# Kernel optimization log

Hardware: AMD Instinct MI355X
Metric: run time of the kernel (lower is better)

Reference implementation:

```python
import jax, jax.numpy as jnp
import numpy as np

BN_EPS = 1e-5


def setup_inputs() -> dict:
    key = jax.random.key(0)
    ks = jax.random.split(key, 16)
    N, E = 50000, 800000
    IN, OUT, EA, EE = 128, 128, 32, 16
    s = lambda k, fi, fo: jax.random.normal(k, (fi, fo), jnp.float32) / np.sqrt(fi)
    return {
        "x": jax.random.normal(ks[0], (N, IN), jnp.float32),
        "edge_attr": jax.random.normal(ks[1], (E, EA), jnp.float32),
        "W_emb": s(ks[2], EA, EE), "b_emb": jnp.zeros((EE,), jnp.float32),
        "W_temb": s(ks[3], EE, OUT), "b_temb": jnp.zeros((OUT,), jnp.float32),
        "W_tattr": s(ks[4], EA, OUT), "b_tattr": jnp.zeros((OUT,), jnp.float32),
        "W_gate": s(ks[5], 3 * OUT, OUT), "b_gate": jnp.zeros((OUT,), jnp.float32),
        "W_l": s(ks[6], IN, OUT), "b_l": jnp.zeros((OUT,), jnp.float32),
        "W_r": s(ks[7], IN, OUT),
        "gamma": jnp.ones((OUT,), jnp.float32), "beta": jnp.zeros((OUT,), jnp.float32),
        "edge_index": jax.random.randint(ks[8], (2, E), 0, N, jnp.int64 if jax.config.jax_enable_x64 else jnp.int32),
    }


def reference(x, edge_attr, W_emb, b_emb, W_temb, b_temb, W_tattr, b_tattr,
              W_gate, b_gate, W_l, b_l, W_r, gamma, beta, edge_index):
    N = x.shape[0]
    row, col = edge_index[0], edge_index[1]

    # edge feature transforms
    emb = jax.nn.relu(edge_attr @ W_emb + b_emb)          # [E, EE]
    t_attr = edge_attr @ W_tattr + b_tattr                # [E, OUT]
    t = (emb @ W_temb + b_temb) + t_attr                  # [E, OUT]

    # SAGEConv (PyG default): mean-aggregate source feats x[row] at target col
    agg = jax.ops.segment_sum(x[row], col, num_segments=N)           # [N, IN]
    cnt = jax.ops.segment_sum(jnp.ones_like(col, x.dtype), col, num_segments=N)
    agg = agg / jnp.maximum(cnt, 1.0)[:, None]
    out = agg @ W_l + b_l + x @ W_r                       # [N, OUT]

    # edge gating: gather out at targets, gate, scatter-add back
    comb = jnp.concatenate([out[col], t, t_attr], axis=-1)  # [E, 3*OUT]
    gate = jax.nn.sigmoid(comb @ W_gate + b_gate)           # [E, OUT]
    out = out + jax.ops.segment_sum(gate * t, col, num_segments=N)

    # BatchNorm1d (training-mode batch stats, biased variance)
    mu = jnp.mean(out, axis=0)
    var = jnp.mean((out - mu) ** 2, axis=0)
    out = (out - mu) * jax.lax.rsqrt(var + BN_EPS) * gamma + beta

    # residual = Identity -> out + out, then relu
    return jax.nn.relu(2.0 * out)
```

## Files before the change

kernel.cpp:

```cpp
#include <hip/hip_runtime.h>
#include <math.h>

#define BN_EPS 1e-5f

typedef short s16x8 __attribute__((ext_vector_type(8)));
typedef float f32x4 __attribute__((ext_vector_type(4)));
#define MFMA16(a, b, c) __builtin_amdgcn_mfma_f32_16x16x32_bf16(a, b, c, 0, 0, 0)

static __device__ __forceinline__ short f2b(float f) {
  union { float f; unsigned u; } x;
  x.f = f;
  unsigned r = (x.u + 0x7fffu + ((x.u >> 16) & 1u)) >> 16;
  return (short)r;
}
static __device__ __forceinline__ float b2f(unsigned bits16) {
  union { unsigned u; float f; } x;
  x.u = bits16 << 16;
  return x.f;
}

__global__ __launch_bounds__(256) void k_prep(
    const float* __restrict__ We, const float* __restrict__ Wta,
    const float* __restrict__ Wte, const float* __restrict__ Wg,
    const float* __restrict__ bta, const float* __restrict__ bte,
    const float* __restrict__ bg,
    short* __restrict__ WembT, short* __restrict__ WtaT,
    short* __restrict__ WteT, short* __restrict__ B1,
    short* __restrict__ B23, short* __restrict__ Bem,
    float* __restrict__ bgf) {
  int t = blockIdx.x * 256 + threadIdx.x;
  if (t < 512) {
    int c = t >> 5, k = t & 31;
    WembT[t] = f2b(We[k * 16 + c]);
  }
  if (t < 4096) {
    int c = t >> 5, k = t & 31;
    WtaT[t] = f2b(Wta[k * 128 + c]);
    WteT[t] = (k < 16) ? f2b(Wte[k * 128 + c]) : (short)0;
  }
  if (t < 16384) {
    int c = t >> 7, k = t & 127;
    B1[t] = f2b(Wg[k * 128 + c]);
    B23[t] = f2b(Wg[(128 + k) * 128 + c] + Wg[(256 + k) * 128 + c]);
  }
  if (t < 4096) {
    int c = t >> 5, k = t & 31;
    float s = 0.f;
    if (k < 16)
      for (int j = 0; j < 128; ++j) s += Wte[k * 128 + j] * Wg[(128 + j) * 128 + c];
    Bem[t] = (k < 16) ? f2b(s) : (short)0;
  }
  if (t < 128) {
    float s = bg[t];
    for (int j = 0; j < 128; ++j)
      s += (bta[j] + bte[j]) * Wg[(128 + j) * 128 + t] +
           bta[j] * Wg[(256 + j) * 128 + t];
    bgf[t] = s;
  }
}

__global__ __launch_bounds__(256) void k_count(
    const int* __restrict__ ei, int* __restrict__ cnt, int E) {
  for (int e = blockIdx.x * blockDim.x + threadIdx.x; e < E;
       e += gridDim.x * blockDim.x)
    atomicAdd(&cnt[ei[E + e]], 1);
}

__global__ __launch_bounds__(1024) void k_scan(
    const int* __restrict__ cnt, int* __restrict__ rowptr,
    int* __restrict__ wo, int N) {
  __shared__ int s[1024];
  __shared__ int carry_s;
  int tid = threadIdx.x;
  if (tid == 0) { carry_s = 0; rowptr[0] = 0; }
  __syncthreads();
  for (int base = 0; base < N; base += 1024) {
    int i = base + tid;
    int v = (i < N) ? cnt[i] : 0;
    s[tid] = v;
    __syncthreads();
#pragma unroll
    for (int off = 1; off < 1024; off <<= 1) {
      int t = (tid >= off) ? s[tid - off] : 0;
      __syncthreads();
      s[tid] += t;
      __syncthreads();
    }
    int inc = s[tid] + carry_s;
    if (i < N) { rowptr[i + 1] = inc; wo[i] = inc - v; }
    __syncthreads();
    if (tid == 1023) carry_s = inc;
    __syncthreads();
  }
}

__global__ __launch_bounds__(256) void k_fill(
    const int* __restrict__ ei, int* __restrict__ wo,
    int* __restrict__ src, int* __restrict__ inv, int E) {
  for (int e = blockIdx.x * blockDim.x + threadIdx.x; e < E;
       e += gridDim.x * blockDim.x) {
    int c = ei[E + e];
    int p = atomicAdd(&wo[c], 1);
    src[p] = ei[e];
    inv[e] = p;
  }
}

__global__ __launch_bounds__(256) void k_agg_gather(
    const float* __restrict__ x, const int* __restrict__ rowptr,
    const int* __restrict__ src, float* __restrict__ agg, int N) {
  int node = blockIdx.x * 4 + (threadIdx.x >> 6);
  if (node >= N) return;
  int l = threadIdx.x & 63;
  int s0 = rowptr[node], s1 = rowptr[node + 1];
  float a0 = 0.f, a1 = 0.f;
  int i = s0;
  for (; i + 1 < s1; i += 2) {
    int sa = src[i], sb = src[i + 1];
    float2 va = reinterpret_cast<const float2*>(x + (size_t)sa * 128)[l];
    float2 vb = reinterpret_cast<const float2*>(x + (size_t)sb * 128)[l];
    a0 += va.x + vb.x;
    a1 += va.y + vb.y;
  }
  if (i < s1) {
    float2 va = reinterpret_cast<const float2*>(x + (size_t)src[i] * 128)[l];
    a0 += va.x;
    a1 += va.y;
  }
  float sc = 1.0f / fmaxf((float)(s1 - s0), 1.0f);
  float2 r = make_float2(a0 * sc, a1 * sc);
  reinterpret_cast<float2*>(agg + (size_t)node * 128)[l] = r;
}

__global__ __launch_bounds__(256) void k_aggregate(
    const float* __restrict__ x, const int* __restrict__ ei,
    float* __restrict__ agg, float* __restrict__ cnt, int N, int E) {
  int total = E * 32;
  for (int idx = blockIdx.x * blockDim.x + threadIdx.x; idx < total;
       idx += gridDim.x * blockDim.x) {
    int e = idx >> 5, c = idx & 31;
    int r = ei[e];
    int d = ei[E + e];
    float4 v = reinterpret_cast<const float4*>(x)[(size_t)r * 32 + c];
    float* dst = agg + (size_t)d * 128 + c * 4;
    unsafeAtomicAdd(dst + 0, v.x);
    unsafeAtomicAdd(dst + 1, v.y);
    unsafeAtomicAdd(dst + 2, v.z);
    unsafeAtomicAdd(dst + 3, v.w);
    if (c == 0) unsafeAtomicAdd(cnt + d, 1.0f);
  }
}

__global__ __launch_bounds__(256) void k_node_linear(
    const float* __restrict__ x, float* __restrict__ agg,
    const float* __restrict__ cntf, const float* __restrict__ Wl,
    const float* __restrict__ bl, const float* __restrict__ Wr,
    float* __restrict__ out_lin, int N, int csr) {
  __shared__ float a_s[32][128];
  __shared__ float x_s[32][128];
  int n0 = blockIdx.x * 32;
  int tid = threadIdx.x;
#pragma unroll
  for (int i = 0; i < 16; ++i) {
    int idx = tid + i * 256;
    int nl = idx >> 7, j = idx & 127;
    int n = n0 + nl;
    float av = 0.f, xv = 0.f;
    if (n < N) {
      size_t off = (size_t)n * 128 + j;
      if (csr) {
        av = agg[off];
      } else {
        av = agg[off] / fmaxf(cntf[n], 1.0f);
        agg[off] = 0.0f;
      }
      xv = x[off];
    }
    a_s[nl][j] = av;
    x_s[nl][j] = xv;
  }
  __syncthreads();
  int j = tid & 127, g = tid >> 7;
  float acc[16];
  float bj = bl[j];
#pragma unroll
  for (int i = 0; i < 16; ++i) acc[i] = bj;
  for (int k = 0; k < 128; ++k) {
    float wl = Wl[k * 128 + j];
    float wr = Wr[k * 128 + j];
#pragma unroll
    for (int i = 0; i < 16; ++i)
      acc[i] += a_s[g * 16 + i][k] * wl + x_s[g * 16 + i][k] * wr;
  }
#pragma unroll
  for (int i = 0; i < 16; ++i) {
    int n = n0 + g * 16 + i;
    if (n < N) out_lin[(size_t)n * 128 + j] = acc[i];
  }
}

template <int MODE>
__global__ __launch_bounds__(256, 4) void k_edge_gate_mfma(
    const float* __restrict__ edge_attr, const int* __restrict__ ei,
    const float* __restrict__ out_lin,
    const short* __restrict__ WembT, const float* __restrict__ b_emb,
    const short* __restrict__ WteT, const float* __restrict__ b_temb,
    const short* __restrict__ WtaT, const float* __restrict__ b_tattr,
    const short* __restrict__ B1, const short* __restrict__ B23,
    const short* __restrict__ Bem, const float* __restrict__ bgf,
    float* __restrict__ acc_out, short* __restrict__ et,
    const int* __restrict__ inv, int E) {
  __shared__ short emb_s[64][40];
  __shared__ short comb_s[64][132];
  __shared__ int col_s[64];
  __shared__ int inv_s[64];

  const int tid = threadIdx.x;
  const int w = tid >> 6;
  const int l = tid & 63;
  const int m = l & 15;
  const int g = l >> 4;
  const int e0 = blockIdx.x * 64;
  const int erow = w * 16;

  if (l < 16) {
    col_s[erow + l] = ei[E + e0 + erow + l];
    if (MODE == 1) inv_s[erow + l] = inv[e0 + erow + l];
  }
  {
    int rr = erow + (l >> 2);
    int cc = 16 + (l & 3) * 4;
    int2 zz = make_int2(0, 0);
    *reinterpret_cast<int2*>(&emb_s[rr][cc]) = zz;
  }

  const f32x4 zf = {0.f, 0.f, 0.f, 0.f};

  s16x8 Aea;
  {
    const float* eap = edge_attr + (size_t)(e0 + erow + m) * 32 + g * 8;
    float4 u0 = *reinterpret_cast<const float4*>(eap);
    float4 u1 = *reinterpret_cast<const float4*>(eap + 4);
    Aea[0] = f2b(u0.x); Aea[1] = f2b(u0.y); Aea[2] = f2b(u0.z); Aea[3] = f2b(u0.w);
    Aea[4] = f2b(u1.x); Aea[5] = f2b(u1.y); Aea[6] = f2b(u1.z); Aea[7] = f2b(u1.w);
  }

  {
    s16x8 Bemb = *reinterpret_cast<const s16x8*>(WembT + m * 32 + g * 8);
    f32x4 Demb = MFMA16(Aea, Bemb, zf);
    float be = b_emb[m];
#pragma unroll
    for (int r = 0; r < 4; ++r)
      emb_s[erow + g * 4 + r][m] = f2b(fmaxf(Demb[r] + be, 0.f));
  }

  s16x8 Aemb = *reinterpret_cast<const s16x8*>(&emb_s[erow + m][g * 8]);

  f32x4 ta[8], tt[8];
#pragma unroll
  for (int n = 0; n < 8; ++n) {
    s16x8 B = *reinterpret_cast<const s16x8*>(WtaT + (n * 16 + m) * 32 + g * 8);
    ta[n] = MFMA16(Aea, B, zf);
  }
#pragma unroll
  for (int n = 0; n < 8; ++n) {
    s16x8 B = *reinterpret_cast<const s16x8*>(WteT + (n * 16 + m) * 32 + g * 8);
    tt[n] = MFMA16(Aemb, B, ta[n]);
  }
#pragma unroll
  for (int n = 0; n < 8; ++n) {
    float bta_ = b_tattr[n * 16 + m];
    float bte_ = b_temb[n * 16 + m];
#pragma unroll
    for (int r = 0; r < 4; ++r) {
      comb_s[erow + g * 4 + r][n * 16 + m] = f2b(ta[n][r]);
      tt[n][r] = tt[n][r] + bta_ + bte_;
    }
  }

  s16x8 Ago[4];
  {
    int cd = col_s[erow + m];
    const float* op = out_lin + (size_t)cd * 128 + g * 8;
#pragma unroll
    for (int kc = 0; kc < 4; ++kc) {
      float4 v0 = *reinterpret_cast<const float4*>(op + kc * 32);
      float4 v1 = *reinterpret_cast<const float4*>(op + kc * 32 + 4);
      s16x8 a;
      a[0] = f2b(v0.x); a[1] = f2b(v0.y); a[2] = f2b(v0.z); a[3] = f2b(v0.w);
      a[4] = f2b(v1.x); a[5] = f2b(v1.y); a[6] = f2b(v1.z); a[7] = f2b(v1.w);
      Ago[kc] = a;
    }
  }
  s16x8 Agt[4];
#pragma unroll
  for (int kc = 0; kc < 4; ++kc)
    Agt[kc] = *reinterpret_cast<const s16x8*>(&comb_s[erow + m][kc * 32 + g * 8]);

  int dD[4];
#pragma unroll
  for (int r = 0; r < 4; ++r)
    dD[r] = (MODE == 1) ? inv_s[erow + g * 4 + r] : col_s[erow + g * 4 + r];

#pragma unroll
  for (int n = 0; n < 8; ++n) {
    const short* b1p = B1 + (n * 16 + m) * 128 + g * 8;
    const short* b23p = B23 + (n * 16 + m) * 128 + g * 8;
    f32x4 acc = zf;
#pragma unroll
    for (int kc = 0; kc < 4; ++kc)
      acc = MFMA16(Ago[kc], *reinterpret_cast<const s16x8*>(b1p + kc * 32), acc);
#pragma unroll
    for (int kc = 0; kc < 4; ++kc)
      acc = MFMA16(Agt[kc], *reinterpret_cast<const s16x8*>(b23p + kc * 32), acc);
    acc = MFMA16(Aemb, *reinterpret_cast<const s16x8*>(Bem + (n * 16 + m) * 32 + g * 8), acc);
    float bg_ = bgf[n * 16 + m];
#pragma unroll
    for (int r = 0; r < 4; ++r) {
      float gate = 1.f / (1.f + __expf(-(acc[r] + bg_)));
      float val = gate * tt[n][r];
      if (MODE == 1) {
        et[(size_t)dD[r] * 128 + n * 16 + m] = f2b(val);
      } else {
        unsafeAtomicAdd(acc_out + (size_t)dD[r] * 128 + n * 16 + m, val);
      }
    }
  }
}

__global__ __launch_bounds__(256) void k_gate_gather(
    const short* __restrict__ et, const int* __restrict__ rowptr,
    float* __restrict__ out, int N) {
  int node = blockIdx.x * 4 + (threadIdx.x >> 6);
  if (node >= N) return;
  int l = threadIdx.x & 63;
  int s0 = rowptr[node], s1 = rowptr[node + 1];
  float a0 = 0.f, a1 = 0.f;
  const unsigned* ep = reinterpret_cast<const unsigned*>(et);
  int i = s0;
  for (; i + 1 < s1; i += 2) {
    unsigned ua = ep[(size_t)i * 64 + l];
    unsigned ub = ep[(size_t)(i + 1) * 64 + l];
    a0 += b2f(ua & 0xffffu) + b2f(ub & 0xffffu);
    a1 += b2f(ua >> 16) + b2f(ub >> 16);
  }
  if (i < s1) {
    unsigned ua = ep[(size_t)i * 64 + l];
    a0 += b2f(ua & 0xffffu);
    a1 += b2f(ua >> 16);
  }
  float2* op = reinterpret_cast<float2*>(out + (size_t)node * 128);
  float2 v = op[l];
  v.x += a0;
  v.y += a1;
  op[l] = v;
}

__global__ __launch_bounds__(256) void k_bn_stats(
    const float* __restrict__ out_lin, const float* __restrict__ acc,
    float* __restrict__ bn, int N) {
  int j = threadIdx.x & 127;
  int g = threadIdx.x >> 7;
  float s = 0.f, s2 = 0.f;
  for (int n = blockIdx.x * 2 + g; n < N; n += gridDim.x * 2) {
    size_t off = (size_t)n * 128 + j;
    float v = out_lin[off];
    if (acc) v += acc[off];
    s += v;
    s2 += v * v;
  }
  unsafeAtomicAdd(&bn[j], s);
  unsafeAtomicAdd(&bn[128 + j], s2);
}

__global__ __launch_bounds__(256) void k_finalize(
    float* __restrict__ out, const float* __restrict__ acc,
    const float* __restrict__ bn, const float* __restrict__ gamma,
    const float* __restrict__ beta, int N) {
  int total = N * 32;
  float invN = 1.0f / (float)N;
  for (int idx = blockIdx.x * blockDim.x + threadIdx.x; idx < total;
       idx += gridDim.x * blockDim.x) {
    int q = idx & 31;
    float4 v = reinterpret_cast<float4*>(out)[idx];
    float4 a = acc ? reinterpret_cast<const float4*>(acc)[idx]
                   : make_float4(0.f, 0.f, 0.f, 0.f);
    float* vp = &v.x;
    const float* ap = &a.x;
    float4 r;
    float* rp = &r.x;
#pragma unroll
    for (int c = 0; c < 4; ++c) {
      int j = q * 4 + c;
      float mu = bn[j] * invN;
      float var = bn[128 + j] * invN - mu * mu;
      float val = vp[c] + ap[c];
      float y = (val - mu) * rsqrtf(var + BN_EPS) * gamma[j] + beta[j];
      rp[c] = fmaxf(2.f * y, 0.f);
    }
    reinterpret_cast<float4*>(out)[idx] = r;
  }
}

extern "C" void kernel_launch(void* const* d_in, const int* in_sizes, int n_in,
                              void* d_out, int out_size, void* d_ws, size_t ws_size,
                              hipStream_t stream) {
  const float* x       = (const float*)d_in[0];
  const float* ea      = (const float*)d_in[1];
  const float* W_emb   = (const float*)d_in[2];
  const float* b_emb   = (const float*)d_in[3];
  const float* W_temb  = (const float*)d_in[4];
  const float* b_temb  = (const float*)d_in[5];
  const float* W_tattr = (const float*)d_in[6];
  const float* b_tattr = (const float*)d_in[7];
  const float* W_gate  = (const float*)d_in[8];
  const float* b_gate  = (const float*)d_in[9];
  const float* W_l     = (const float*)d_in[10];
  const float* b_l     = (const float*)d_in[11];
  const float* W_r     = (const float*)d_in[12];
  const float* gamma   = (const float*)d_in[13];
  const float* beta    = (const float*)d_in[14];
  const int*   eidx    = (const int*)d_in[15];

  int N = in_sizes[0] / 128;
  int E = in_sizes[1] / 32;
  float* out = (float*)d_out;
  char* base = (char*)d_ws;

  const size_t WB_SHORTS = 512 + 4096 + 4096 + 16384 + 16384 + 4096;

  size_t o = 0;
  auto take = [&](size_t b) { size_t r = o; o = (o + b + 255) & ~(size_t)255; return r; };
  size_t o_agg    = take((size_t)N * 128 * 4);
  size_t o_cnt    = take((size_t)N * 4);
  size_t o_rowptr = take((size_t)(N + 1) * 4);
  size_t o_wo     = take((size_t)N * 4);
  size_t o_src    = take((size_t)E * 4);
  size_t o_inv    = take((size_t)E * 4);
  size_t o_bn     = take(256 * 4);
  size_t o_wb     = take(WB_SHORTS * 2);
  size_t o_bgf    = take(128 * 4);
  size_t o_et     = take((size_t)E * 128 * 2);
  bool csr = (ws_size >= o);

  if (csr) {
    float* agg    = (float*)(base + o_agg);
    int*   cnt    = (int*)(base + o_cnt);
    int*   rowptr = (int*)(base + o_rowptr);
    int*   wo     = (int*)(base + o_wo);
    int*   src    = (int*)(base + o_src);
    int*   inv    = (int*)(base + o_inv);
    float* bn     = (float*)(base + o_bn);
    short* wb     = (short*)(base + o_wb);
    short* WembT  = wb;
    short* WtaT   = wb + 512;
    short* WteT   = wb + 4608;
    short* B1     = wb + 8704;
    short* B23    = wb + 25088;
    short* Bem    = wb + 41472;
    float* bgf    = (float*)(base + o_bgf);
    short* et     = (short*)(base + o_et);

    hipMemsetAsync(cnt, 0, (size_t)N * 4, stream);
    hipMemsetAsync(bn, 0, 256 * 4, stream);

    k_prep<<<64, 256, 0, stream>>>(W_emb, W_tattr, W_temb, W_gate,
                                   b_tattr, b_temb, b_gate,
                                   WembT, WtaT, WteT, B1, B23, Bem, bgf);
    k_count<<<512, 256, 0, stream>>>(eidx, cnt, E);
    k_scan<<<1, 1024, 0, stream>>>(cnt, rowptr, wo, N);
    k_fill<<<512, 256, 0, stream>>>(eidx, wo, src, inv, E);
    k_agg_gather<<<(N + 3) / 4, 256, 0, stream>>>(x, rowptr, src, agg, N);
    k_node_linear<<<(N + 31) / 32, 256, 0, stream>>>(x, agg, nullptr, W_l, b_l,
                                                     W_r, out, N, 1);
    k_edge_gate_mfma<1><<<E / 64, 256, 0, stream>>>(
        ea, eidx, out, WembT, b_emb, WteT, b_temb, WtaT, b_tattr,
        B1, B23, Bem, bgf, nullptr, et, inv, E);
    k_gate_gather<<<(N + 3) / 4, 256, 0, stream>>>(et, rowptr, out, N);
    k_bn_stats<<<512, 256, 0, stream>>>(out, nullptr, bn, N);
    k_finalize<<<2048, 256, 0, stream>>>(out, nullptr, bn, gamma, beta, N);
  } else {
    float* agg  = (float*)d_ws;
    float* cntf = agg + (size_t)N * 128;
    float* bn   = cntf + N;
    short* wb   = (short*)(bn + 256);
    short* WembT = wb;
    short* WtaT  = wb + 512;
    short* WteT  = wb + 4608;
    short* B1    = wb + 8704;
    short* B23   = wb + 25088;
    short* Bem   = wb + 41472;
    float* bgf   = (float*)(wb + WB_SHORTS + (WB_SHORTS & 1));

    size_t zero_bytes = ((size_t)N * 128 + N + 256) * sizeof(float);
    hipMemsetAsync(d_ws, 0, zero_bytes, stream);

    k_prep<<<64, 256, 0, stream>>>(W_emb, W_tattr, W_temb, W_gate,
                                   b_tattr, b_temb, b_gate,
                                   WembT, WtaT, WteT, B1, B23, Bem, bgf);
    k_aggregate<<<2048, 256, 0, stream>>>(x, eidx, agg, cntf, N, E);
    k_node_linear<<<(N + 31) / 32, 256, 0, stream>>>(x, agg, cntf, W_l, b_l,
                                                     W_r, out, N, 0);
    k_edge_gate_mfma<0><<<E / 64, 256, 0, stream>>>(
        ea, eidx, out, WembT, b_emb, WteT, b_temb, WtaT, b_tattr,
        B1, B23, Bem, bgf, agg, nullptr, nullptr, E);
    k_bn_stats<<<512, 256, 0, stream>>>(out, agg, bn, N);
    k_finalize<<<2048, 256, 0, stream>>>(out, agg, bn, gamma, beta, N);
  }
}
```

Baseline: 1.209 ms.

## Fold t_attr gate weights into edge_attr GEMM and gather bf16 node outputs

Precomputes W_tattr·(W_gate2+W_gate3) so the gate's t_attr contribution becomes one K=32 MFMA on edge_attr rather than four K=128 MFMAs on a staged t_attr tile. This removes the comb_s shared buffer and its LDS traffic. node_linear also writes a bf16 copy of its output, so the edge kernel gathers half the bytes and skips per-element conversion. The occupancy hint is raised to 6 waves per SIMD. In exchange, rounding changes slightly because the fused weight is rounded to bf16 once, and there is an extra bf16 store per node.

```diff
diff --git a/kernel.cpp b/kernel.cpp
--- a/kernel.cpp
+++ b/kernel.cpp
@@ -26,7 +26,7 @@
     const float* __restrict__ bg,
     short* __restrict__ WembT, short* __restrict__ WtaT,
     short* __restrict__ WteT, short* __restrict__ B1,
-    short* __restrict__ B23, short* __restrict__ Bem,
+    short* __restrict__ Bta23, short* __restrict__ Bem,
     float* __restrict__ bgf) {
   int t = blockIdx.x * 256 + threadIdx.x;
   if (t < 512) {
@@ -41,14 +41,18 @@
   if (t < 16384) {
     int c = t >> 7, k = t & 127;
     B1[t] = f2b(Wg[k * 128 + c]);
-    B23[t] = f2b(Wg[(128 + k) * 128 + c] + Wg[(256 + k) * 128 + c]);
   }
   if (t < 4096) {
     int c = t >> 5, k = t & 31;
     float s = 0.f;
+    for (int j = 0; j < 128; ++j)
+      s += Wta[k * 128 + j] *
+           (Wg[(128 + j) * 128 + c] + Wg[(256 + j) * 128 + c]);
+    Bta23[t] = f2b(s);
+    float s2 = 0.f;
     if (k < 16)
-      for (int j = 0; j < 128; ++j) s += Wte[k * 128 + j] * Wg[(128 + j) * 128 + c];
-    Bem[t] = (k < 16) ? f2b(s) : (short)0;
+      for (int j = 0; j < 128; ++j) s2 += Wte[k * 128 + j] * Wg[(128 + j) * 128 + c];
+    Bem[t] = (k < 16) ? f2b(s2) : (short)0;
   }
   if (t < 128) {
     float s = bg[t];
@@ -155,7 +159,7 @@
     const float* __restrict__ x, float* __restrict__ agg,
     const float* __restrict__ cntf, const float* __restrict__ Wl,
     const float* __restrict__ bl, const float* __restrict__ Wr,
-    float* __restrict__ out_lin, int N, int csr) {
+    float* __restrict__ out_lin, short* __restrict__ obf, int N, int csr) {
   __shared__ float a_s[32][128];
   __shared__ float x_s[32][128];
   int n0 = blockIdx.x * 32;
@@ -195,23 +199,26 @@
 #pragma unroll
   for (int i = 0; i < 16; ++i) {
     int n = n0 + g * 16 + i;
-    if (n < N) out_lin[(size_t)n * 128 + j] = acc[i];
+    if (n < N) {
+      size_t off = (size_t)n * 128 + j;
+      out_lin[off] = acc[i];
+      if (obf) obf[off] = f2b(acc[i]);
+    }
   }
 }
 
 template <int MODE>
-__global__ __launch_bounds__(256, 4) void k_edge_gate_mfma(
+__global__ __launch_bounds__(256, 6) void k_edge_gate_mfma(
     const float* __restrict__ edge_attr, const int* __restrict__ ei,
-    const float* __restrict__ out_lin,
+    const float* __restrict__ out_lin, const short* __restrict__ obf,
     const short* __restrict__ WembT, const float* __restrict__ b_emb,
     const short* __restrict__ WteT, const float* __restrict__ b_temb,
     const short* __restrict__ WtaT, const float* __restrict__ b_tattr,
-    const short* __restrict__ B1, const short* __restrict__ B23,
+    const short* __restrict__ B1, const short* __restrict__ Bta23,
     const short* __restrict__ Bem, const float* __restrict__ bgf,
     float* __restrict__ acc_out, short* __restrict__ et,
     const int* __restrict__ inv, int E) {
   __shared__ short emb_s[64][40];
-  __shared__ short comb_s[64][132];
   __shared__ int col_s[64];
   __shared__ int inv_s[64];
 
@@ -256,46 +263,42 @@
 
   s16x8 Aemb = *reinterpret_cast<const s16x8*>(&emb_s[erow + m][g * 8]);
 
-  f32x4 ta[8], tt[8];
+  f32x4 tt[8];
 #pragma unroll
   for (int n = 0; n < 8; ++n) {
     s16x8 B = *reinterpret_cast<const s16x8*>(WtaT + (n * 16 + m) * 32 + g * 8);
-    ta[n] = MFMA16(Aea, B, zf);
+    f32x4 ta = MFMA16(Aea, B, zf);
+    s16x8 B2 = *reinterpret_cast<const s16x8*>(WteT + (n * 16 + m) * 32 + g * 8);
+    tt[n] = MFMA16(Aemb, B2, ta);
   }
 #pragma unroll
   for (int n = 0; n < 8; ++n) {
-    s16x8 B = *reinterpret_cast<const s16x8*>(WteT + (n * 16 + m) * 32 + g * 8);
-    tt[n] = MFMA16(Aemb, B, ta[n]);
-  }
-#pragma unroll
-  for (int n = 0; n < 8; ++n) {
-    float bta_ = b_tattr[n * 16 + m];
-    float bte_ = b_temb[n * 16 + m];
-#pragma unroll
-    for (int r = 0; r < 4; ++r) {
-      comb_s[erow + g * 4 + r][n * 16 + m] = f2b(ta[n][r]);
-      tt[n][r] = tt[n][r] + bta_ + bte_;
-    }
+    float badd = b_tattr[n * 16 + m] + b_temb[n * 16 + m];
+#pragma unroll
+    for (int r = 0; r < 4; ++r) tt[n][r] += badd;
   }
 
   s16x8 Ago[4];
   {
     int cd = col_s[erow + m];
-    const float* op = out_lin + (size_t)cd * 128 + g * 8;
-#pragma unroll
-    for (int kc = 0; kc < 4; ++kc) {
-      float4 v0 = *reinterpret_cast<const float4*>(op + kc * 32);
-      float4 v1 = *reinterpret_cast<const float4*>(op + kc * 32 + 4);
-      s16x8 a;
-      a[0] = f2b(v0.x); a[1] = f2b(v0.y); a[2] = f2b(v0.z); a[3] = f2b(v0.w);
-      a[4] = f2b(v1.x); a[5] = f2b(v1.y); a[6] = f2b(v1.z); a[7] = f2b(v1.w);
-      Ago[kc] = a;
+    if (MODE == 1) {
+      const short* op = obf + (size_t)cd * 128 + g * 8;
+#pragma unroll
+      for (int kc = 0; kc < 4; ++kc)
+        Ago[kc] = *reinterpret_cast<const s16x8*>(op + kc * 32);
+    } else {
+      const float* op = out_lin + (size_t)cd * 128 + g * 8;
+#pragma unroll
+      for (int kc = 0; kc < 4; ++kc) {
+        float4 v0 = *reinterpret_cast<const float4*>(op + kc * 32);
+        float4 v1 = *reinterpret_cast<const float4*>(op + kc * 32 + 4);
+        s16x8 a;
+        a[0] = f2b(v0.x); a[1] = f2b(v0.y); a[2] = f2b(v0.z); a[3] = f2b(v0.w);
+        a[4] = f2b(v1.x); a[5] = f2b(v1.y); a[6] = f2b(v1.z); a[7] = f2b(v1.w);
+        Ago[kc] = a;
+      }
     }
   }
-  s16x8 Agt[4];
-#pragma unroll
-  for (int kc = 0; kc < 4; ++kc)
-    Agt[kc] = *reinterpret_cast<const s16x8*>(&comb_s[erow + m][kc * 32 + g * 8]);
 
   int dD[4];
 #pragma unroll
@@ -305,14 +308,11 @@
 #pragma unroll
   for (int n = 0; n < 8; ++n) {
     const short* b1p = B1 + (n * 16 + m) * 128 + g * 8;
-    const short* b23p = B23 + (n * 16 + m) * 128 + g * 8;
     f32x4 acc = zf;
 #pragma unroll
     for (int kc = 0; kc < 4; ++kc)
       acc = MFMA16(Ago[kc], *reinterpret_cast<const s16x8*>(b1p + kc * 32), acc);
-#pragma unroll
-    for (int kc = 0; kc < 4; ++kc)
-      acc = MFMA16(Agt[kc], *reinterpret_cast<const s16x8*>(b23p + kc * 32), acc);
+    acc = MFMA16(Aea, *reinterpret_cast<const s16x8*>(Bta23 + (n * 16 + m) * 32 + g * 8), acc);
     acc = MFMA16(Aemb, *reinterpret_cast<const s16x8*>(Bem + (n * 16 + m) * 32 + g * 8), acc);
     float bg_ = bgf[n * 16 + m];
 #pragma unroll
@@ -427,11 +427,12 @@
   float* out = (float*)d_out;
   char* base = (char*)d_ws;
 
-  const size_t WB_SHORTS = 512 + 4096 + 4096 + 16384 + 16384 + 4096;
+  const size_t WB_SHORTS = 512 + 4096 + 4096 + 16384 + 4096 + 4096;
 
   size_t o = 0;
   auto take = [&](size_t b) { size_t r = o; o = (o + b + 255) & ~(size_t)255; return r; };
   size_t o_agg    = take((size_t)N * 128 * 4);
+  size_t o_obf    = take((size_t)N * 128 * 2);
   size_t o_cnt    = take((size_t)N * 4);
   size_t o_rowptr = take((size_t)(N + 1) * 4);
   size_t o_wo     = take((size_t)N * 4);
@@ -445,6 +446,7 @@
 
   if (csr) {
     float* agg    = (float*)(base + o_agg);
+    short* obf    = (short*)(base + o_obf);
     int*   cnt    = (int*)(base + o_cnt);
     int*   rowptr = (int*)(base + o_rowptr);
     int*   wo     = (int*)(base + o_wo);
@@ -456,8 +458,8 @@
     short* WtaT   = wb + 512;
     short* WteT   = wb + 4608;
     short* B1     = wb + 8704;
-    short* B23    = wb + 25088;
-    short* Bem    = wb + 41472;
+    short* Bta23  = wb + 25088;
+    short* Bem    = wb + 29184;
     float* bgf    = (float*)(base + o_bgf);
     short* et     = (short*)(base + o_et);
 
@@ -466,16 +468,16 @@
 
     k_prep<<<64, 256, 0, stream>>>(W_emb, W_tattr, W_temb, W_gate,
                                    b_tattr, b_temb, b_gate,
-                                   WembT, WtaT, WteT, B1, B23, Bem, bgf);
+                                   WembT, WtaT, WteT, B1, Bta23, Bem, bgf);
     k_count<<<512, 256, 0, stream>>>(eidx, cnt, E);
     k_scan<<<1, 1024, 0, stream>>>(cnt, rowptr, wo, N);
     k_fill<<<512, 256, 0, stream>>>(eidx, wo, src, inv, E);
     k_agg_gather<<<(N + 3) / 4, 256, 0, stream>>>(x, rowptr, src, agg, N);
     k_node_linear<<<(N + 31) / 32, 256, 0, stream>>>(x, agg, nullptr, W_l, b_l,
-                                                     W_r, out, N, 1);
+                                                     W_r, out, obf, N, 1);
     k_edge_gate_mfma<1><<<E / 64, 256, 0, stream>>>(
-        ea, eidx, out, WembT, b_emb, WteT, b_temb, WtaT, b_tattr,
-        B1, B23, Bem, bgf, nullptr, et, inv, E);
+        ea, eidx, out, obf, WembT, b_emb, WteT, b_temb, WtaT, b_tattr,
+        B1, Bta23, Bem, bgf, nullptr, et, inv, E);
     k_gate_gather<<<(N + 3) / 4, 256, 0, stream>>>(et, rowptr, out, N);
     k_bn_stats<<<512, 256, 0, stream>>>(out, nullptr, bn, N);
     k_finalize<<<2048, 256, 0, stream>>>(out, nullptr, bn, gamma, beta, N);
@@ -488,8 +490,8 @@
     short* WtaT  = wb + 512;
     short* WteT  = wb + 4608;
     short* B1    = wb + 8704;
-    short* B23   = wb + 25088;
-    short* Bem   = wb + 41472;
+    short* Bta23 = wb + 25088;
+    short* Bem   = wb + 29184;
     float* bgf   = (float*)(wb + WB_SHORTS + (WB_SHORTS & 1));
 
     size_t zero_bytes = ((size_t)N * 128 + N + 256) * sizeof(float);
@@ -497,13 +499,13 @@
 
     k_prep<<<64, 256, 0, stream>>>(W_emb, W_tattr, W_temb, W_gate,
                                    b_tattr, b_temb, b_gate,
-                                   WembT, WtaT, WteT, B1, B23, Bem, bgf);
+                                   WembT, WtaT, WteT, B1, Bta23, Bem, bgf);
     k_aggregate<<<2048, 256, 0, stream>>>(x, eidx, agg, cntf, N, E);
     k_node_linear<<<(N + 31) / 32, 256, 0, stream>>>(x, agg, cntf, W_l, b_l,
-                                                     W_r, out, N, 0);
+                                                     W_r, out, nullptr, N, 0);
     k_edge_gate_mfma<0><<<E / 64, 256, 0, stream>>>(
-        ea, eidx, out, WembT, b_emb, WteT, b_temb, WtaT, b_tattr,
-        B1, B23, Bem, bgf, agg, nullptr, nullptr, E);
+        ea, eidx, out, nullptr, WembT, b_emb, WteT, b_temb, WtaT, b_tattr,
+        B1, Bta23, Bem, bgf, agg, nullptr, nullptr, E);
     k_bn_stats<<<512, 256, 0, stream>>>(out, agg, bn, N);
     k_finalize<<<2048, 256, 0, stream>>>(out, agg, bn, gamma, beta, N);
   }
```

Measured after the change: 1.048 ms. 1.15x faster.
